# Optimization experiments

Measured on AMD Instinct MI355X. Metric: run time of the kernel, lower is better.

## Reference

```python
import jax, jax.numpy as jnp
import numpy as np

SHAPE = (64, 64, 64, 16)
RANK = 8


def tr_to_matrix(factors, in_dim):
    # Tensor-ring reconstruction: T[i1..id] = trace(G1[:,i1,:] @ ... @ Gd[:,id,:])
    acc = factors[0]  # (r, n0, r)
    for f in factors[1:]:
        r = acc.shape[0]
        acc = jnp.einsum('amb,bnc->amnc', acc, f).reshape(r, -1, r)
    # close the ring with a trace over the boundary rank
    full = jnp.trace(acc, axis1=0, axis2=2)  # (prod(SHAPE),)
    return full.reshape(in_dim, -1)


def setup_inputs() -> dict:
    key = jax.random.key(0)
    ks = jax.random.split(key, 5)
    x = jax.random.normal(ks[0], (8192, 2048), dtype=jnp.float32)
    factors = {}
    for i, n in enumerate(SHAPE):
        factors[f'f{i}'] = jax.random.uniform(
            ks[i + 1], (RANK, n, RANK), dtype=jnp.float32, minval=-0.1, maxval=0.1)
    return {'x': x, **factors}


def reference(x, f0, f1, f2, f3):
    W = tr_to_matrix([f0, f1, f2, f3], x.shape[1])  # (2048, 2048)
    return jnp.matmul(x, W)
```

## Files before the change

kernel.cpp:

```cpp
#include <hip/hip_runtime.h>
#include <hip/hip_bf16.h>
#include <stdint.h>

typedef unsigned short u16;
typedef __attribute__((ext_vector_type(8))) unsigned short u16x8;
typedef __attribute__((ext_vector_type(8))) __bf16 bf16x8;
typedef __attribute__((ext_vector_type(4))) float f32x4;

__device__ __forceinline__ u16 f2bf(float f) {
    uint32_t u = __builtin_bit_cast(uint32_t, f);
    u = (u + 0x7fffu + ((u >> 16) & 1u)) >> 16;
    return (u16)u;
}

__device__ __forceinline__ float bf2f(u16 v) {
    return __builtin_bit_cast(float, (uint32_t)v << 16);
}

__device__ __forceinline__ bf16x8 cvt8(const float* p) {
    f32x4 a = *(const f32x4*)p;
    f32x4 b = *(const f32x4*)(p + 4);
    u16x8 o;
    o[0] = f2bf(a[0]); o[1] = f2bf(a[1]); o[2] = f2bf(a[2]); o[3] = f2bf(a[3]);
    o[4] = f2bf(b[0]); o[5] = f2bf(b[1]); o[6] = f2bf(b[2]); o[7] = f2bf(b[3]);
    return __builtin_bit_cast(bf16x8, o);
}

__global__ __launch_bounds__(256) void prep_kernel(const float* __restrict__ f0,
                                                   const float* __restrict__ f1,
                                                   const float* __restrict__ f2,
                                                   const float* __restrict__ f3,
                                                   u16* __restrict__ H12bT,
                                                   u16* __restrict__ H34T) {
    int gid = blockIdx.x * 256 + threadIdx.x;
    if (gid < 262144) {
        int rc = gid >> 11;
        int k  = gid & 2047;
        int p = rc >> 6, e = rc & 63;
        int a = e >> 3, b = e & 7;
        int i1 = k >> 5, i2 = ((k & 31) << 1) | p;
        float s = 0.f;
#pragma unroll
        for (int m = 0; m < 8; m++)
            s += f0[a * 512 + i1 * 8 + m] * f1[m * 512 + i2 * 8 + b];
        H12bT[gid] = f2bf(s);
    } else {
        int g = gid - 262144;
        int c = g >> 6;
        int e = g & 63;
        int a = e >> 3, b = e & 7;
        int i3 = c >> 4, i4 = c & 15;
        float s = 0.f;
#pragma unroll
        for (int cc = 0; cc < 8; cc++)
            s += f2[b * 512 + i3 * 8 + cc] * f3[cc * 128 + i4 * 8 + a];
        H34T[c * 64 + e] = f2bf(s);
    }
}

__global__ __launch_bounds__(256) void k1_kernel(const float* __restrict__ x,
                                                 const u16* __restrict__ H12bT,
                                                 u16* __restrict__ Ypb) {
    int tid = threadIdx.x, lane = tid & 63, w = tid >> 6;
    int lm = lane & 15, lkE = (lane >> 4) << 3;
    int r0 = blockIdx.x * 256 + w * 64;
    int k0 = blockIdx.y * 256;

    f32x4 acc[4][8];
#pragma unroll
    for (int s = 0; s < 4; ++s)
#pragma unroll
        for (int j = 0; j < 8; ++j) acc[s][j] = (f32x4){0.f, 0.f, 0.f, 0.f};

    const float* xB = x + (size_t)(r0 + lm) * 2048 + k0 + lkE;
    const u16*  bP  = H12bT + (size_t)lm * 2048 + k0 + lkE;

#pragma unroll
    for (int kc = 0; kc < 8; ++kc) {
        int ko = kc * 32;
        bf16x8 a[4];
#pragma unroll
        for (int s = 0; s < 4; ++s)
            a[s] = cvt8(xB + (size_t)(s * 16) * 2048 + ko);
        bf16x8 bf[8];
#pragma unroll
        for (int j = 0; j < 8; ++j)
            bf[j] = __builtin_bit_cast(bf16x8, *(const u16x8*)(bP + (size_t)j * 16 * 2048 + ko));
#pragma unroll
        for (int j = 0; j < 8; ++j)
#pragma unroll
            for (int s = 0; s < 4; ++s)
                acc[s][j] = __builtin_amdgcn_mfma_f32_16x16x32_bf16(a[s], bf[j], acc[s][j], 0, 0, 0);
    }
    u16* ywB = Ypb + (size_t)blockIdx.y * 1048576 + (size_t)(r0 + ((lane >> 4) << 2)) * 128 + lm;
#pragma unroll
    for (int s = 0; s < 4; ++s)
#pragma unroll
        for (int j = 0; j < 8; ++j) {
            f32x4 v = acc[s][j];
#pragma unroll
            for (int r = 0; r < 4; ++r)
                ywB[(size_t)(s * 16 + r) * 128 + j * 16] = f2bf(v[r]);
        }
}

__global__ __launch_bounds__(512) void k2r_kernel(const u16* __restrict__ Ypb,
                                                  const u16* __restrict__ H34T,
                                                  float* __restrict__ out) {
    __shared__ u16 Yl[32][136];
    int tid = threadIdx.x, lane = tid & 63, w = tid >> 6;
    int lm = lane & 15, lkE = (lane >> 4) << 3;
    int r0 = blockIdx.x * 32;

    {
        int row0 = tid >> 4;
        int ce = (tid & 15) << 3;
        float s0[8];
#pragma unroll
        for (int e = 0; e < 8; ++e) s0[e] = 0.f;
#pragma unroll
        for (int ks = 0; ks < 8; ++ks) {
            const u16* b = Ypb + (size_t)ks * 1048576 + (size_t)(r0 + row0) * 128 + ce;
            u16x8 v = *(const u16x8*)b;
#pragma unroll
            for (int e = 0; e < 8; ++e) s0[e] += bf2f(v[e]);
        }
        u16x8 o;
#pragma unroll
        for (int e = 0; e < 8; ++e) o[e] = f2bf(s0[e]);
        *(u16x8*)&Yl[row0][ce] = o;
    }
    __syncthreads();

    int p = w >> 2, ch = (w & 3) << 8;
    bf16x8 ya[2][2];
#pragma unroll
    for (int rh = 0; rh < 2; ++rh)
#pragma unroll
        for (int kc = 0; kc < 2; ++kc)
            ya[rh][kc] = __builtin_bit_cast(bf16x8,
                *(const u16x8*)&Yl[rh * 16 + lm][p * 64 + kc * 32 + lkE]);

    const u16* hB = H34T + (size_t)(ch + lm) * 64 + lkE;
    float* cW = out + (size_t)(r0 + ((lane >> 4) << 2)) * 2048 + (w << 8) + lm;

#pragma unroll 4
    for (int cf = 0; cf < 16; ++cf) {
        const u16* hr = hB + (size_t)cf * 1024;
        bf16x8 h0 = __builtin_bit_cast(bf16x8, *(const u16x8*)(hr));
        bf16x8 h1 = __builtin_bit_cast(bf16x8, *(const u16x8*)(hr + 32));
        f32x4 a0 = (f32x4){0.f, 0.f, 0.f, 0.f};
        f32x4 a1 = (f32x4){0.f, 0.f, 0.f, 0.f};
        a0 = __builtin_amdgcn_mfma_f32_16x16x32_bf16(ya[0][0], h0, a0, 0, 0, 0);
        a0 = __builtin_amdgcn_mfma_f32_16x16x32_bf16(ya[0][1], h1, a0, 0, 0, 0);
        a1 = __builtin_amdgcn_mfma_f32_16x16x32_bf16(ya[1][0], h0, a1, 0, 0, 0);
        a1 = __builtin_amdgcn_mfma_f32_16x16x32_bf16(ya[1][1], h1, a1, 0, 0, 0);
#pragma unroll
        for (int r = 0; r < 4; ++r) {
            cW[(size_t)r * 2048 + cf * 16] = a0[r];
            cW[(size_t)(16 + r) * 2048 + cf * 16] = a1[r];
        }
    }
}

extern "C" void kernel_launch(void* const* d_in, const int* in_sizes, int n_in,
                              void* d_out, int out_size, void* d_ws, size_t ws_size,
                              hipStream_t stream) {
    const float* x  = (const float*)d_in[0];
    const float* f0 = (const float*)d_in[1];
    const float* f1 = (const float*)d_in[2];
    const float* f2 = (const float*)d_in[3];
    const float* f3 = (const float*)d_in[4];
    float* out = (float*)d_out;

    char* ws = (char*)d_ws;
    u16* H12bT = (u16*)ws;
    u16* H34T  = (u16*)(ws + (512u << 10));
    u16* Ypb   = (u16*)(ws + (1u << 20));
    if (ws_size < ((size_t)18 << 20)) return;

    prep_kernel<<<1280, 256, 0, stream>>>(f0, f1, f2, f3, H12bT, H34T);
    k1_kernel<<<dim3(32, 8), 256, 0, stream>>>(x, H12bT, Ypb);
    k2r_kernel<<<256, 512, 0, stream>>>(Ypb, H34T, out);
}
```

Baseline: 49.70 us.

## Double-buffer k1 global loads with inline asm and explicit vmcnt waits

```diff
diff --git a/kernel.cpp b/kernel.cpp
--- a/kernel.cpp
+++ b/kernel.cpp
@@ -15,15 +15,6 @@
 
 __device__ __forceinline__ float bf2f(u16 v) {
     return __builtin_bit_cast(float, (uint32_t)v << 16);
-}
-
-__device__ __forceinline__ bf16x8 cvt8(const float* p) {
-    f32x4 a = *(const f32x4*)p;
-    f32x4 b = *(const f32x4*)(p + 4);
-    u16x8 o;
-    o[0] = f2bf(a[0]); o[1] = f2bf(a[1]); o[2] = f2bf(a[2]); o[3] = f2bf(a[3]);
-    o[4] = f2bf(b[0]); o[5] = f2bf(b[1]); o[6] = f2bf(b[2]); o[7] = f2bf(b[3]);
-    return __builtin_bit_cast(bf16x8, o);
 }
 
 __global__ __launch_bounds__(256) void prep_kernel(const float* __restrict__ f0,
@@ -58,9 +49,9 @@
     }
 }
 
-__global__ __launch_bounds__(256) void k1_kernel(const float* __restrict__ x,
-                                                 const u16* __restrict__ H12bT,
-                                                 u16* __restrict__ Ypb) {
+__global__ __launch_bounds__(256, 1) void k1_kernel(const float* __restrict__ x,
+                                                    const u16* __restrict__ H12bT,
+                                                    u16* __restrict__ Ypb) {
     int tid = threadIdx.x, lane = tid & 63, w = tid >> 6;
     int lm = lane & 15, lkE = (lane >> 4) << 3;
     int r0 = blockIdx.x * 256 + w * 64;
@@ -72,26 +63,67 @@
 #pragma unroll
         for (int j = 0; j < 8; ++j) acc[s][j] = (f32x4){0.f, 0.f, 0.f, 0.f};
 
-    const float* xB = x + (size_t)(r0 + lm) * 2048 + k0 + lkE;
-    const u16*  bP  = H12bT + (size_t)lm * 2048 + k0 + lkE;
-
-#pragma unroll
-    for (int kc = 0; kc < 8; ++kc) {
-        int ko = kc * 32;
-        bf16x8 a[4];
-#pragma unroll
-        for (int s = 0; s < 4; ++s)
-            a[s] = cvt8(xB + (size_t)(s * 16) * 2048 + ko);
-        bf16x8 bf[8];
-#pragma unroll
-        for (int j = 0; j < 8; ++j)
-            bf[j] = __builtin_bit_cast(bf16x8, *(const u16x8*)(bP + (size_t)j * 16 * 2048 + ko));
-#pragma unroll
-        for (int j = 0; j < 8; ++j)
-#pragma unroll
-            for (int s = 0; s < 4; ++s)
-                acc[s][j] = __builtin_amdgcn_mfma_f32_16x16x32_bf16(a[s], bf[j], acc[s][j], 0, 0, 0);
-    }
+    const float* xS[4];
+    const u16*   bJ[8];
+#pragma unroll
+    for (int s = 0; s < 4; ++s)
+        xS[s] = x + (size_t)(r0 + s * 16 + lm) * 2048 + k0 + lkE;
+#pragma unroll
+    for (int j = 0; j < 8; ++j)
+        bJ[j] = H12bT + (size_t)(j * 16 + lm) * 2048 + k0 + lkE;
+
+    f32x4 xa[2][4][2];
+    u16x8 bb[2][8];
+
+#define ISSUE(set_, kc_) do { \
+    _Pragma("unroll") \
+    for (int s = 0; s < 4; ++s) { \
+        asm volatile("global_load_dwordx4 %0, %1, off" \
+                     : "=v"(xa[set_][s][0]) : "v"(xS[s] + (kc_) * 32)); \
+        asm volatile("global_load_dwordx4 %0, %1, off" \
+                     : "=v"(xa[set_][s][1]) : "v"(xS[s] + (kc_) * 32 + 4)); \
+    } \
+    _Pragma("unroll") \
+    for (int j = 0; j < 8; ++j) { \
+        asm volatile("global_load_dwordx4 %0, %1, off" \
+                     : "=v"(bb[set_][j]) : "v"(bJ[j] + (kc_) * 32)); \
+    } \
+} while (0)
+
+#define STEP(kc_, set_, nset_, WAITN) do { \
+    if ((kc_) < 7) ISSUE(nset_, (kc_) + 1); \
+    asm volatile("s_waitcnt vmcnt(" #WAITN ")" ::: "memory"); \
+    __builtin_amdgcn_sched_barrier(0); \
+    bf16x8 a_[4]; \
+    _Pragma("unroll") \
+    for (int s = 0; s < 4; ++s) { \
+        f32x4 A0 = xa[set_][s][0], A1 = xa[set_][s][1]; \
+        u16x8 o; \
+        o[0] = f2bf(A0[0]); o[1] = f2bf(A0[1]); o[2] = f2bf(A0[2]); o[3] = f2bf(A0[3]); \
+        o[4] = f2bf(A1[0]); o[5] = f2bf(A1[1]); o[6] = f2bf(A1[2]); o[7] = f2bf(A1[3]); \
+        a_[s] = __builtin_bit_cast(bf16x8, o); \
+    } \
+    _Pragma("unroll") \
+    for (int j = 0; j < 8; ++j) { \
+        bf16x8 bfj = __builtin_bit_cast(bf16x8, bb[set_][j]); \
+        _Pragma("unroll") \
+        for (int s = 0; s < 4; ++s) \
+            acc[s][j] = __builtin_amdgcn_mfma_f32_16x16x32_bf16(a_[s], bfj, acc[s][j], 0, 0, 0); \
+    } \
+} while (0)
+
+    ISSUE(0, 0);
+    STEP(0, 0, 1, 16);
+    STEP(1, 1, 0, 16);
+    STEP(2, 0, 1, 16);
+    STEP(3, 1, 0, 16);
+    STEP(4, 0, 1, 16);
+    STEP(5, 1, 0, 16);
+    STEP(6, 0, 1, 16);
+    STEP(7, 1, 0, 0);
+#undef ISSUE
+#undef STEP
+
     u16* ywB = Ypb + (size_t)blockIdx.y * 1048576 + (size_t)(r0 + ((lane >> 4) << 2)) * 128 + lm;
 #pragma unroll
     for (int s = 0; s < 4; ++s)
```

Measured after the change: 47.61 us. -4.2%, faster.
